# Kernel optimization log

Measured on AMD Instinct MI355X. Metric: run time of the kernel, lower is better.

Reference implementation:

```python
import jax, jax.numpy as jnp
import numpy as np

H, M = 1024, 8
HM = H * M
DT, TM, TA, TZI, TZJ, TP = 0.001, 0.05, 2.7, 0.24, 0.24, 10.0
EPS = np.float32(np.finfo(np.float32).tiny)


def log_eps(x):
    return jnp.log(jnp.where(x <= 0.0, EPS, x))


def setup_inputs() -> dict:
    key = jax.random.key(0)
    ks = jax.random.split(key, 13)
    f32 = jnp.float32
    return {
        "x": jax.random.uniform(ks[0], (H, M), f32),
        "s": jax.random.normal(ks[1], (H, M), f32),
        "o": jax.random.uniform(ks[2], (H, M), f32),
        "a": jax.random.normal(ks[3], (H, M), f32) * 0.1,
        "zi": jax.random.uniform(ks[4], (H, M), f32),
        "zj": jax.random.uniform(ks[5], (H, M), f32),
        "p": jax.random.uniform(ks[6], (), f32),
        "pi": jax.random.uniform(ks[7], (H, M), f32),
        "pj": jax.random.uniform(ks[8], (H, M), f32),
        "pij": jax.random.uniform(ks[9], (HM, HM), f32),
        "b": jax.random.normal(ks[10], (H, M), f32),
        "w": jax.random.normal(ks[11], (HM, HM), f32) * 0.01,
        "noise": jax.random.normal(ks[12], (H, M), f32),
        "ga": jnp.float32(1.0),
        "gw": jnp.float32(1.0),
        "gb": jnp.float32(1.0),
        "gs": jnp.float32(0.1),
        "k": jnp.float32(1.0),
    }


def reference(x, s, o, a, zi, zj, p, pi, pj, pij, b, w, noise, ga, gw, gb, gs, k):
    # --- update_state (train=True uses gw) ---
    st = gw * (b.reshape(-1) + w.T @ o.reshape(-1))          # GEMV, [HM]
    s_new = s + DT / TM * (st.reshape(H, M) - a + log_eps(x) + gs * noise - s)
    o_new = jax.nn.softmax(s_new, axis=1)
    a_new = a + DT / TA * (ga * o_new - a)
    # --- update_traces ---
    zi_new = zi + DT / TZI * (o_new - zi)
    zj_new = zj + DT / TZJ * (o_new - zj)
    # --- update_probabilities ---
    c = k * DT / TP
    p_new = p + c * (1.0 - p)
    pi_new = pi + c * (zi_new - pi)
    pj_new = pj + c * (zj_new - pj)
    pij_new = pij + c * (jnp.outer(zi_new.reshape(-1), zj_new.reshape(-1)) - pij)
    # --- update_connections ---
    w_new = log_eps(p_new * pij_new / jnp.outer(pi_new.reshape(-1), pj_new.reshape(-1)))
    b_new = gb * log_eps(pj_new)
    # torch forward returns o (buffers updated in place); JAX returns full new state
    return (o_new, s_new, a_new, zi_new, zj_new, p_new, pi_new, pj_new, pij_new, w_new, b_new)
```

## Files before the change

### kernel.cpp

```cpp
#include <hip/hip_runtime.h>
#include <math.h>

#define H_N 1024
#define M_N 8
#define HM 8192

static __device__ __forceinline__ float log_eps(float x) {
    const float EPS_TINY = 1.17549435e-38f;
    return __logf(x <= 0.0f ? EPS_TINY : x);
}

__global__ __launch_bounds__(256) void gemv_partial(const float* __restrict__ w,
                                                    const float* __restrict__ o,
                                                    float* __restrict__ st_acc) {
    const int jb = blockIdx.x & 7;
    const int ic = blockIdx.x >> 3;
    const int j0 = jb * 1024 + threadIdx.x * 4;
    const int i0 = ic * 128;
    float ax = 0.f, ay = 0.f, az = 0.f, aw = 0.f;
    const float* wp = w + (size_t)i0 * HM + j0;
#pragma unroll 4
    for (int i = 0; i < 128; ++i) {
        const float ov = o[i0 + i];
        const float4 wv = *reinterpret_cast<const float4*>(wp);
        ax += wv.x * ov; ay += wv.y * ov; az += wv.z * ov; aw += wv.w * ov;
        wp += HM;
    }
    atomicAdd(&st_acc[j0 + 0], ax);
    atomicAdd(&st_acc[j0 + 1], ay);
    atomicAdd(&st_acc[j0 + 2], az);
    atomicAdd(&st_acc[j0 + 3], aw);
}

__global__ __launch_bounds__(256) void row_kernel(
    const float* __restrict__ x, const float* __restrict__ s,
    const float* __restrict__ a, const float* __restrict__ zi,
    const float* __restrict__ zj, const float* __restrict__ p,
    const float* __restrict__ pi, const float* __restrict__ pj,
    const float* __restrict__ b, const float* __restrict__ noise,
    const float* __restrict__ ga, const float* __restrict__ gw,
    const float* __restrict__ gb, const float* __restrict__ gs,
    const float* __restrict__ k, const float* __restrict__ st_acc,
    float* __restrict__ out) {
    const int r = blockIdx.x * blockDim.x + threadIdx.x;
    if (r >= H_N) return;

    const float gwv = gw[0], gav = ga[0], gbv = gb[0], gsv = gs[0], kv = k[0], pv = p[0];
    const float c = kv * 0.001f / 10.0f;

    float* o_new  = out;
    float* s_new  = out + (size_t)HM;
    float* a_new  = out + (size_t)2 * HM;
    float* zi_new = out + (size_t)3 * HM;
    float* zj_new = out + (size_t)4 * HM;
    float* p_new  = out + (size_t)5 * HM;
    float* pi_new = out + (size_t)5 * HM + 1;
    float* pj_new = out + (size_t)6 * HM + 1;
    float* b_new  = out + (size_t)7 * HM + 1 + (size_t)2 * HM * HM;

    const int base = r * M_N;
    float sv[M_N], ev[M_N];
    float mx = -3.0e38f;
#pragma unroll
    for (int m = 0; m < M_N; ++m) {
        const int i = base + m;
        const float st = gwv * (b[i] + st_acc[i]);
        const float sn = s[i] + 0.02f * (st - a[i] + log_eps(x[i]) + gsv * noise[i] - s[i]);
        sv[m] = sn;
        mx = fmaxf(mx, sn);
    }
    float sum = 0.f;
#pragma unroll
    for (int m = 0; m < M_N; ++m) { ev[m] = __expf(sv[m] - mx); sum += ev[m]; }
    const float rs = 1.0f / sum;
#pragma unroll
    for (int m = 0; m < M_N; ++m) {
        const int i = base + m;
        const float on  = ev[m] * rs;
        const float an  = a[i]  + (float)(0.001 / 2.7)  * (gav * on - a[i]);
        const float zin = zi[i] + (float)(0.001 / 0.24) * (on - zi[i]);
        const float zjn = zj[i] + (float)(0.001 / 0.24) * (on - zj[i]);
        const float pin = pi[i] + c * (zin - pi[i]);
        const float pjn = pj[i] + c * (zjn - pj[i]);
        o_new[i]  = on;
        s_new[i]  = sv[m];
        a_new[i]  = an;
        zi_new[i] = zin;
        zj_new[i] = zjn;
        pi_new[i] = pin;
        pj_new[i] = pjn;
        b_new[i]  = gbv * log_eps(pjn);
    }
    if (r == 0) p_new[0] = pv + c * (1.0f - pv);
}

__global__ __launch_bounds__(256) void outer_kernel(
    const float* __restrict__ pij, const float* __restrict__ out_ro,
    float* __restrict__ out, const float* __restrict__ p,
    const float* __restrict__ k) {
    const float* zi_new = out_ro + (size_t)3 * HM;
    const float* zj_new = out_ro + (size_t)4 * HM;
    const float* pi_new = out_ro + (size_t)5 * HM + 1;
    const float* pj_new = out_ro + (size_t)6 * HM + 1;
    float* pij_new = out + (size_t)7 * HM + 1;
    float* w_new   = pij_new + (size_t)HM * HM;

    const float kv = k[0], pv = p[0];
    const float c  = kv * 0.001f / 10.0f;
    const float pn = pv + c * (1.0f - pv);

    const size_t nvec   = (size_t)HM * HM / 4;
    const size_t stride = (size_t)gridDim.x * blockDim.x;
    for (size_t v = (size_t)blockIdx.x * blockDim.x + threadIdx.x; v < nvec; v += stride) {
        const size_t idx = v * 4;
        const int I = (int)(idx >> 13);
        const int J = (int)(idx & 8191);
        const float ziI = zi_new[I];
        const float piI = pi_new[I];
        const float4 pv4 = *reinterpret_cast<const float4*>(&pij[idx]);
        const float zj0 = zj_new[J + 0], zj1 = zj_new[J + 1], zj2 = zj_new[J + 2], zj3 = zj_new[J + 3];
        const float pj0 = pj_new[J + 0], pj1 = pj_new[J + 1], pj2 = pj_new[J + 2], pj3 = pj_new[J + 3];

        const float q0 = pv4.x + c * (ziI * zj0 - pv4.x);
        const float q1 = pv4.y + c * (ziI * zj1 - pv4.y);
        const float q2 = pv4.z + c * (ziI * zj2 - pv4.z);
        const float q3 = pv4.w + c * (ziI * zj3 - pv4.w);

        pij_new[idx + 0] = q0;
        pij_new[idx + 1] = q1;
        pij_new[idx + 2] = q2;
        pij_new[idx + 3] = q3;

        const float v0 = __fdividef(pn * q0, piI * pj0);
        const float v1 = __fdividef(pn * q1, piI * pj1);
        const float v2 = __fdividef(pn * q2, piI * pj2);
        const float v3 = __fdividef(pn * q3, piI * pj3);

        w_new[idx + 0] = log_eps(v0);
        w_new[idx + 1] = log_eps(v1);
        w_new[idx + 2] = log_eps(v2);
        w_new[idx + 3] = log_eps(v3);
    }
}

extern "C" void kernel_launch(void* const* d_in, const int* in_sizes, int n_in,
                              void* d_out, int out_size, void* d_ws, size_t ws_size,
                              hipStream_t stream) {
    const float* x     = (const float*)d_in[0];
    const float* s     = (const float*)d_in[1];
    const float* o     = (const float*)d_in[2];
    const float* a     = (const float*)d_in[3];
    const float* zi    = (const float*)d_in[4];
    const float* zj    = (const float*)d_in[5];
    const float* p     = (const float*)d_in[6];
    const float* pi    = (const float*)d_in[7];
    const float* pj    = (const float*)d_in[8];
    const float* pij   = (const float*)d_in[9];
    const float* b     = (const float*)d_in[10];
    const float* w     = (const float*)d_in[11];
    const float* noise = (const float*)d_in[12];
    const float* ga    = (const float*)d_in[13];
    const float* gw    = (const float*)d_in[14];
    const float* gb    = (const float*)d_in[15];
    const float* gs    = (const float*)d_in[16];
    const float* k     = (const float*)d_in[17];

    float* out = (float*)d_out;
    float* st_acc = (float*)d_ws;

    hipMemsetAsync(st_acc, 0, HM * sizeof(float), stream);
    gemv_partial<<<512, 256, 0, stream>>>(w, o, st_acc);
    row_kernel<<<(H_N + 255) / 256, 256, 0, stream>>>(
        x, s, a, zi, zj, p, pi, pj, b, noise, ga, gw, gb, gs, k, st_acc, out);
    outer_kernel<<<2048, 256, 0, stream>>>(pij, out, out, p, k);
}
```

Before: 268.5 us.

## Realign outer-product stores to 16B boundary with shifted vector window and nontemporal stores

```diff
diff --git a/kernel.cpp b/kernel.cpp
--- a/kernel.cpp
+++ b/kernel.cpp
@@ -4,6 +4,8 @@
 #define H_N 1024
 #define M_N 8
 #define HM 8192
+
+typedef float f32x4 __attribute__((ext_vector_type(4)));
 
 static __device__ __forceinline__ float log_eps(float x) {
     const float EPS_TINY = 1.17549435e-38f;
@@ -22,7 +24,7 @@
 #pragma unroll 4
     for (int i = 0; i < 128; ++i) {
         const float ov = o[i0 + i];
-        const float4 wv = *reinterpret_cast<const float4*>(wp);
+        const f32x4 wv = *reinterpret_cast<const f32x4*>(wp);
         ax += wv.x * ov; ay += wv.y * ov; az += wv.z * ov; aw += wv.w * ov;
         wp += HM;
     }
@@ -46,7 +48,7 @@
     if (r >= H_N) return;
 
     const float gwv = gw[0], gav = ga[0], gbv = gb[0], gsv = gs[0], kv = k[0], pv = p[0];
-    const float c = kv * 0.001f / 10.0f;
+    const float c = kv * 1e-4f;
 
     float* o_new  = out;
     float* s_new  = out + (size_t)HM;
@@ -106,40 +108,73 @@
     float* w_new   = pij_new + (size_t)HM * HM;
 
     const float kv = k[0], pv = p[0];
-    const float c  = kv * 0.001f / 10.0f;
+    const float c  = kv * 1e-4f;
     const float pn = pv + c * (1.0f - pv);
 
-    const size_t nvec   = (size_t)HM * HM / 4;
+    const size_t N  = (size_t)HM * HM;
+    const size_t NQ = N / 4 - 1;
     const size_t stride = (size_t)gridDim.x * blockDim.x;
-    for (size_t v = (size_t)blockIdx.x * blockDim.x + threadIdx.x; v < nvec; v += stride) {
-        const size_t idx = v * 4;
-        const int I = (int)(idx >> 13);
-        const int J = (int)(idx & 8191);
-        const float ziI = zi_new[I];
-        const float piI = pi_new[I];
-        const float4 pv4 = *reinterpret_cast<const float4*>(&pij[idx]);
-        const float zj0 = zj_new[J + 0], zj1 = zj_new[J + 1], zj2 = zj_new[J + 2], zj3 = zj_new[J + 3];
-        const float pj0 = pj_new[J + 0], pj1 = pj_new[J + 1], pj2 = pj_new[J + 2], pj3 = pj_new[J + 3];
-
-        const float q0 = pv4.x + c * (ziI * zj0 - pv4.x);
-        const float q1 = pv4.y + c * (ziI * zj1 - pv4.y);
-        const float q2 = pv4.z + c * (ziI * zj2 - pv4.z);
-        const float q3 = pv4.w + c * (ziI * zj3 - pv4.w);
-
-        pij_new[idx + 0] = q0;
-        pij_new[idx + 1] = q1;
-        pij_new[idx + 2] = q2;
-        pij_new[idx + 3] = q3;
-
-        const float v0 = __fdividef(pn * q0, piI * pj0);
-        const float v1 = __fdividef(pn * q1, piI * pj1);
-        const float v2 = __fdividef(pn * q2, piI * pj2);
-        const float v3 = __fdividef(pn * q3, piI * pj3);
-
-        w_new[idx + 0] = log_eps(v0);
-        w_new[idx + 1] = log_eps(v1);
-        w_new[idx + 2] = log_eps(v2);
-        w_new[idx + 3] = log_eps(v3);
+    size_t t = (size_t)blockIdx.x * blockDim.x + threadIdx.x;
+
+    if (t == 0) {
+        const float zi0 = zi_new[0], pi0 = pi_new[0];
+#pragma unroll
+        for (int e = 0; e < 3; ++e) {
+            const float pe = pij[e];
+            const float q  = pe + c * (zi0 * zj_new[e] - pe);
+            pij_new[e] = q;
+            w_new[e]   = log_eps(__fdividef(pn * q, pi0 * pj_new[e]));
+        }
+        const size_t eN = N - 1;
+        const float pe = pij[eN];
+        const float q  = pe + c * (zi_new[HM - 1] * zj_new[HM - 1] - pe);
+        pij_new[eN] = q;
+        w_new[eN]   = log_eps(__fdividef(pn * q, pi_new[HM - 1] * pj_new[HM - 1]));
+    }
+
+    const f32x4* pij4 = reinterpret_cast<const f32x4*>(pij);
+    for (; t < NQ; t += stride) {
+        const size_t e0 = 4 * t + 3;
+        const f32x4 A = pij4[t];
+        const f32x4 B = pij4[t + 1];
+        const float p0 = A.w, p1 = B.x, p2 = B.y, p3 = B.z;
+
+        float q0, q1, q2, q3, w0, w1, w2, w3;
+        const int J0 = (int)(e0 & (HM - 1));
+        if (J0 != HM - 1) {
+            const int I = (int)(e0 >> 13);
+            const float ziI = zi_new[I];
+            const float piI = pi_new[I];
+            const float zj0 = zj_new[J0], zj1 = zj_new[J0 + 1], zj2 = zj_new[J0 + 2], zj3 = zj_new[J0 + 3];
+            const float pj0 = pj_new[J0], pj1 = pj_new[J0 + 1], pj2 = pj_new[J0 + 2], pj3 = pj_new[J0 + 3];
+            q0 = p0 + c * (ziI * zj0 - p0);
+            q1 = p1 + c * (ziI * zj1 - p1);
+            q2 = p2 + c * (ziI * zj2 - p2);
+            q3 = p3 + c * (ziI * zj3 - p3);
+            w0 = log_eps(__fdividef(pn * q0, piI * pj0));
+            w1 = log_eps(__fdividef(pn * q1, piI * pj1));
+            w2 = log_eps(__fdividef(pn * q2, piI * pj2));
+            w3 = log_eps(__fdividef(pn * q3, piI * pj3));
+        } else {
+            float pv4[4] = {p0, p1, p2, p3};
+            float qq[4], ww[4];
+#pragma unroll
+            for (int m = 0; m < 4; ++m) {
+                const size_t e = e0 + m;
+                const int Im = (int)(e >> 13);
+                const int Jm = (int)(e & (HM - 1));
+                const float q = pv4[m] + c * (zi_new[Im] * zj_new[Jm] - pv4[m]);
+                qq[m] = q;
+                ww[m] = log_eps(__fdividef(pn * q, pi_new[Im] * pj_new[Jm]));
+            }
+            q0 = qq[0]; q1 = qq[1]; q2 = qq[2]; q3 = qq[3];
+            w0 = ww[0]; w1 = ww[1]; w2 = ww[2]; w3 = ww[3];
+        }
+
+        f32x4 Q; Q.x = q0; Q.y = q1; Q.z = q2; Q.w = q3;
+        f32x4 W; W.x = w0; W.y = w1; W.z = w2; W.w = w3;
+        __builtin_nontemporal_store(Q, reinterpret_cast<f32x4*>(&pij_new[e0]));
+        __builtin_nontemporal_store(W, reinterpret_cast<f32x4*>(&w_new[e0]));
     }
 }
 
@@ -168,9 +203,9 @@
     float* out = (float*)d_out;
     float* st_acc = (float*)d_ws;
 
-    hipMemsetAsync(st_acc, 0, HM * sizeof(float), stream);
+    (void)hipMemsetAsync(st_acc, 0, HM * sizeof(float), stream);
     gemv_partial<<<512, 256, 0, stream>>>(w, o, st_acc);
     row_kernel<<<(H_N + 255) / 256, 256, 0, stream>>>(
         x, s, a, zi, zj, p, pi, pj, b, noise, ga, gw, gb, gs, k, st_acc, out);
-    outer_kernel<<<2048, 256, 0, stream>>>(pij, out, out, p, k);
-}
+    outer_kernel<<<4096, 256, 0, stream>>>(pij, out, out, p, k);
+}
```

Result: slower. 297.5 us (+10.8%).
